# Performance work log

Measured on AMD Instinct MI355X. Metric: run time of the kernel, lower is better.

## Reference

```python
import jax, jax.numpy as jnp
import numpy as np

N, NFEAT, NHID, NCLASS, NHEAD = 8192, 512, 64, 16, 4
ALPHA = 0.1  # leaky relu slope
NEG = -9e15


def setup_inputs() -> dict:
    key = jax.random.key(0)
    ks = jax.random.split(key, 7)
    x = jax.random.normal(ks[0], (N, NFEAT), dtype=jnp.float32)
    adj = (jax.random.uniform(ks[1], (N, N)) < 0.05).astype(jnp.float32)
    # per-head params: W [H, nfeat, nhid], a [H, 2*nhid] (xavier-ish scale)
    W = jax.random.normal(ks[2], (NHEAD, NFEAT, NHID), dtype=jnp.float32) * (1.0 / np.sqrt(NFEAT))
    a = jax.random.normal(ks[3], (NHEAD, 2 * NHID), dtype=jnp.float32) * (1.0 / np.sqrt(NHID))
    W_out = jax.random.normal(ks[4], (NHEAD * NHID, NCLASS), dtype=jnp.float32) * (1.0 / np.sqrt(NHEAD * NHID))
    a_out = jax.random.normal(ks[5], (2 * NCLASS,), dtype=jnp.float32) * (1.0 / np.sqrt(NCLASS))
    return {"x": x, "adj": adj, "W": W, "a": a, "W_out": W_out, "a_out": a_out}


def _gat_layer(h, adj, Wk, ak):
    """Dense pyGAT GraphAttentionLayer (eval mode, dropout = identity)."""
    d = Wk.shape[1]
    Wh = h @ Wk                         # [N, d]
    f1 = Wh @ ak[:d]                    # [N]
    f2 = Wh @ ak[d:]                    # [N]
    e = jax.nn.leaky_relu(f1[:, None] + f2[None, :], negative_slope=ALPHA)  # [N, N]
    att = jax.nn.softmax(jnp.where(adj > 0, e, NEG), axis=1)
    return att @ Wh                     # [N, d]


def reference(x, adj, W, a, W_out, a_out):
    # eval mode: F.dropout is identity
    heads = jax.vmap(lambda Wk, ak: jax.nn.elu(_gat_layer(x, adj, Wk, ak)))(W, a)  # [H, N, nhid]
    h = jnp.transpose(heads, (1, 0, 2)).reshape(x.shape[0], -1)                    # [N, H*nhid]
    out = jax.nn.elu(_gat_layer(h, adj, W_out, a_out))                             # [N, nclass]
    return jax.nn.log_softmax(out, axis=1)
```

## Files before the change

### kernel.cpp

```cpp
#include <hip/hip_runtime.h>
#include <hip/hip_bf16.h>

#define NN 8192
#define NFEAT 512
#define NHID 64
#define NCLASS 16
#define NHEAD 4
#define ALPHA 0.1f
#define CAP 768

typedef short bf16x8 __attribute__((ext_vector_type(8)));
typedef float f32x4 __attribute__((ext_vector_type(4)));
typedef float fv4 __attribute__((ext_vector_type(4)));

__device__ __forceinline__ float lrelu(float x) { return fmaxf(x, ALPHA * x); }
__device__ __forceinline__ float elu(float x) { return x > 0.f ? x : __expf(x) - 1.f; }
__device__ __forceinline__ short f2b(float x) {
  union { __bf16 b; short s; } c; c.b = (__bf16)x; return c.s;
}
__device__ __forceinline__ float b2f(short x) {
  union { unsigned int u; float f; } c; c.u = ((unsigned int)(unsigned short)x) << 16; return c.f;
}

#define UPF(w, v, A0, A1)                                  \
  {                                                        \
    const float lo_ = __uint_as_float((v) << 16);          \
    const float hi_ = __uint_as_float((v) & 0xffff0000u);  \
    (A0) += (w) * lo_;                                     \
    (A1) += (w) * hi_;                                     \
  }

__global__ __launch_bounds__(256) void k_wprep(const float* __restrict__ W,
                                               short* __restrict__ WB) {
  __shared__ float t[64][65];
  const int h = blockIdx.y;
  const int k0 = blockIdx.x * 64;
  const int tid = threadIdx.x;
#pragma unroll
  for (int it = 0; it < 16; ++it) {
    const int r = it * 4 + (tid >> 6), c = tid & 63;
    t[r][c] = W[((size_t)h * NFEAT + k0 + r) * NHID + c];
  }
  __syncthreads();
#pragma unroll
  for (int it = 0; it < 16; ++it) {
    const int d = it * 4 + (tid >> 6), k = tid & 63;
    WB[((size_t)h * NHID + d) * NFEAT + k0 + k] = f2b(t[k][d]);
  }
}

__global__ __launch_bounds__(256) void k_prep1(const float* __restrict__ x,
                                               const short* __restrict__ WB,
                                               const float* __restrict__ a,
                                               short* __restrict__ WhB,
                                               float* __restrict__ f1i,
                                               float* __restrict__ f2i) {
  __shared__ short tile[64][72];
  const int bid = blockIdx.x;
  const int h = bid >> 7;
  const int bm = (bid & 127) * 64;
  const int tid = threadIdx.x;
  const int wv = tid >> 6, lane = tid & 63;
  const int mr = lane & 15, kg = lane >> 4;
  f32x4 acc0 = {0.f, 0.f, 0.f, 0.f}, acc1 = acc0, acc2 = acc0, acc3 = acc0;
  const float* ap = x + (size_t)(bm + wv * 16 + mr) * NFEAT + kg * 8;
  const short* bp = WB + ((size_t)h * NHID + mr) * NFEAT + kg * 8;
#pragma unroll 2
  for (int k0 = 0; k0 < NFEAT; k0 += 32) {
    const float4 xa = *reinterpret_cast<const float4*>(ap);
    const float4 xb = *reinterpret_cast<const float4*>(ap + 4);
    bf16x8 af;
    af[0] = f2b(xa.x); af[1] = f2b(xa.y); af[2] = f2b(xa.z); af[3] = f2b(xa.w);
    af[4] = f2b(xb.x); af[5] = f2b(xb.y); af[6] = f2b(xb.z); af[7] = f2b(xb.w);
    const bf16x8 b0 = *reinterpret_cast<const bf16x8*>(bp);
    const bf16x8 b1 = *reinterpret_cast<const bf16x8*>(bp + 16 * NFEAT);
    const bf16x8 b2 = *reinterpret_cast<const bf16x8*>(bp + 32 * NFEAT);
    const bf16x8 b3 = *reinterpret_cast<const bf16x8*>(bp + 48 * NFEAT);
    acc0 = __builtin_amdgcn_mfma_f32_16x16x32_bf16(af, b0, acc0, 0, 0, 0);
    acc1 = __builtin_amdgcn_mfma_f32_16x16x32_bf16(af, b1, acc1, 0, 0, 0);
    acc2 = __builtin_amdgcn_mfma_f32_16x16x32_bf16(af, b2, acc2, 0, 0, 0);
    acc3 = __builtin_amdgcn_mfma_f32_16x16x32_bf16(af, b3, acc3, 0, 0, 0);
    ap += 32; bp += 32;
  }
  float a1v[4], a2v[4];
#pragma unroll
  for (int c = 0; c < 4; ++c) {
    a1v[c] = a[h * 128 + mr + c * 16];
    a2v[c] = a[h * 128 + 64 + mr + c * 16];
  }
#pragma unroll
  for (int q = 0; q < 4; ++q) {
    float s1 = acc0[q] * a1v[0] + acc1[q] * a1v[1] + acc2[q] * a1v[2] + acc3[q] * a1v[3];
    float s2 = acc0[q] * a2v[0] + acc1[q] * a2v[1] + acc2[q] * a2v[2] + acc3[q] * a2v[3];
#pragma unroll
    for (int off = 1; off < 16; off <<= 1) {
      s1 += __shfl_xor(s1, off);
      s2 += __shfl_xor(s2, off);
    }
    if (mr == 0) {
      const int i = bm + wv * 16 + kg * 4 + q;
      f1i[(size_t)i * 4 + h] = s1;
      f2i[(size_t)i * 4 + h] = s2;
    }
  }
#pragma unroll
  for (int q = 0; q < 4; ++q) {
    const int r = wv * 16 + kg * 4 + q;
    tile[r][mr +  0] = f2b(acc0[q]);
    tile[r][mr + 16] = f2b(acc1[q]);
    tile[r][mr + 32] = f2b(acc2[q]);
    tile[r][mr + 48] = f2b(acc3[q]);
  }
  __syncthreads();
  {
    const int row = tid >> 2, seg = tid & 3;
    bf16x8 o0, o1;
#pragma unroll
    for (int u = 0; u < 8; ++u) {
      o0[u] = tile[row][seg * 16 + u];
      o1[u] = tile[row][seg * 16 + 8 + u];
    }
    short* dst = WhB + (size_t)(bm + row) * 256 + h * 64 + seg * 16;
    *reinterpret_cast<bf16x8*>(dst) = o0;
    *reinterpret_cast<bf16x8*>(dst + 8) = o1;
  }
}

__global__ __launch_bounds__(256) void k_rmax(const float* __restrict__ src,
                                              float* __restrict__ dst, int n, int stride,
                                              int boff) {
  const float* p = src + (size_t)blockIdx.x * boff;
  float m = -1e30f;
  for (int k = threadIdx.x; k < n; k += 256) m = fmaxf(m, p[(size_t)k * stride]);
#pragma unroll
  for (int off = 32; off; off >>= 1) m = fmaxf(m, __shfl_xor(m, off));
  __shared__ float sm[4];
  if ((threadIdx.x & 63) == 0) sm[threadIdx.x >> 6] = m;
  __syncthreads();
  if (threadIdx.x == 0) dst[blockIdx.x] = fmaxf(fmaxf(sm[0], sm[1]), fmaxf(sm[2], sm[3]));
}

__global__ __launch_bounds__(256) void k_scan(const float* __restrict__ adj,
                                              unsigned int* __restrict__ bmask) {
  const fv4* a4 = reinterpret_cast<const fv4*>(adj);
  const int t0 = blockIdx.x * 256 + threadIdx.x;
#pragma unroll 4
  for (int it = 0; it < 32; ++it) {
    const int g = it * 524288 + t0;
    const fv4 v = __builtin_nontemporal_load(a4 + g);
    unsigned int nv = (unsigned int)((v.x > 0.f) | ((v.y > 0.f) << 1) |
                                     ((v.z > 0.f) << 2) | ((v.w > 0.f) << 3))
                      << ((threadIdx.x & 7) * 4);
    nv |= __shfl_xor(nv, 1);
    nv |= __shfl_xor(nv, 2);
    nv |= __shfl_xor(nv, 4);
    if ((threadIdx.x & 7) == 0) bmask[g >> 3] = nv;
  }
}

__global__ __launch_bounds__(256) void k_attn1b(const unsigned int* __restrict__ bmask,
                                                const short* __restrict__ WhB,
                                                const float* __restrict__ f1i,
                                                const float* __restrict__ f2i,
                                                const float* __restrict__ f2max,
                                                short* __restrict__ hcat) {
  __shared__ unsigned short idx[CAP];
  __shared__ unsigned int widx[NHEAD][CAP + 32];
  __shared__ float swred[4][NHEAD];
  __shared__ float sinv[NHEAD];
  __shared__ int cnt;
  const int i = blockIdx.x;
  const int tid = threadIdx.x;
  const int wv = tid >> 6, lane = tid & 63;
  if (tid == 0) cnt = 0;
  __syncthreads();

  {
    unsigned int word = bmask[(size_t)i * 256 + tid];
    const int c = __popc(word);
    if (c) {
      int base = atomicAdd(&cnt, c);
      const int j0 = tid * 32;
      while (word) {
        const int b = __ffs(word) - 1;
        word &= word - 1;
        if (base < CAP) idx[base++] = (unsigned short)(j0 + b);
      }
    }
  }
  __syncthreads();
  const int n = min(cnt, CAP);

  if (tid < 128) widx[tid >> 5][n + (tid & 31)] = 0;

  const float4 f1v = *reinterpret_cast<const float4*>(f1i + (size_t)i * 4);
  const float4 fmx = *reinterpret_cast<const float4*>(f2max);
  float f1r[4], mrow[4], sw[4] = {0.f, 0.f, 0.f, 0.f};
  f1r[0] = f1v.x; f1r[1] = f1v.y; f1r[2] = f1v.z; f1r[3] = f1v.w;
  mrow[0] = lrelu(f1r[0] + fmx.x);
  mrow[1] = lrelu(f1r[1] + fmx.y);
  mrow[2] = lrelu(f1r[2] + fmx.z);
  mrow[3] = lrelu(f1r[3] + fmx.w);
  const float4* f2i4 = reinterpret_cast<const float4*>(f2i);
  for (int k = tid; k < n; k += 256) {
    const int j = idx[k];
    const float4 f = f2i4[j];
    const float w0 = __expf(lrelu(f1r[0] + f.x) - mrow[0]);
    const float w1 = __expf(lrelu(f1r[1] + f.y) - mrow[1]);
    const float w2 = __expf(lrelu(f1r[2] + f.z) - mrow[2]);
    const float w3 = __expf(lrelu(f1r[3] + f.w) - mrow[3]);
    widx[0][k] = ((unsigned int)(unsigned short)f2b(w0) << 16) | (unsigned int)j;
    widx[1][k] = ((unsigned int)(unsigned short)f2b(w1) << 16) | (unsigned int)j;
    widx[2][k] = ((unsigned int)(unsigned short)f2b(w2) << 16) | (unsigned int)j;
    widx[3][k] = ((unsigned int)(unsigned short)f2b(w3) << 16) | (unsigned int)j;
    sw[0] += w0; sw[1] += w1; sw[2] += w2; sw[3] += w3;
  }
#pragma unroll
  for (int off = 32; off; off >>= 1)
#pragma unroll
    for (int h = 0; h < NHEAD; ++h) sw[h] += __shfl_xor(sw[h], off);
  if (lane == 0) {
#pragma unroll
    for (int h = 0; h < NHEAD; ++h) swred[wv][h] = sw[h];
  }
  __syncthreads();
  if (tid < NHEAD) sinv[tid] = 1.f / (swred[0][tid] + swred[1][tid] + swred[2][tid] + swred[3][tid]);

  const int grp = lane >> 4, l = lane & 15;
  float acc0 = 0.f, acc1 = 0.f, acc2 = 0.f, acc3 = 0.f;
  const short* wb = WhB + wv * 64 + l * 4;
  const unsigned int* wrow = widx[wv];
  __syncthreads();
  for (int kb = grp * 8; kb < n; kb += 32) {
    const uint4 pa = *reinterpret_cast<const uint4*>(wrow + kb);
    const uint4 pb = *reinterpret_cast<const uint4*>(wrow + kb + 4);
    const uint2 e0 = *reinterpret_cast<const uint2*>(wb + (size_t)(pa.x & 0xffffu) * 256);
    const uint2 e1 = *reinterpret_cast<const uint2*>(wb + (size_t)(pa.y & 0xffffu) * 256);
    const uint2 e2 = *reinterpret_cast<const uint2*>(wb + (size_t)(pa.z & 0xffffu) * 256);
    const uint2 e3 = *reinterpret_cast<const uint2*>(wb + (size_t)(pa.w & 0xffffu) * 256);
    const uint2 e4 = *reinterpret_cast<const uint2*>(wb + (size_t)(pb.x & 0xffffu) * 256);
    const uint2 e5 = *reinterpret_cast<const uint2*>(wb + (size_t)(pb.y & 0xffffu) * 256);
    const uint2 e6 = *reinterpret_cast<const uint2*>(wb + (size_t)(pb.z & 0xffffu) * 256);
    const uint2 e7 = *reinterpret_cast<const uint2*>(wb + (size_t)(pb.w & 0xffffu) * 256);
    const float w0 = __uint_as_float(pa.x & 0xffff0000u);
    const float w1 = __uint_as_float(pa.y & 0xffff0000u);
    const float w2 = __uint_as_float(pa.z & 0xffff0000u);
    const float w3 = __uint_as_float(pa.w & 0xffff0000u);
    const float w4 = __uint_as_float(pb.x & 0xffff0000u);
    const float w5 = __uint_as_float(pb.y & 0xffff0000u);
    const float w6 = __uint_as_float(pb.z & 0xffff0000u);
    const float w7 = __uint_as_float(pb.w & 0xffff0000u);
    UPF(w0, e0.x, acc0, acc1) UPF(w0, e0.y, acc2, acc3)
    UPF(w1, e1.x, acc0, acc1) UPF(w1, e1.y, acc2, acc3)
    UPF(w2, e2.x, acc0, acc1) UPF(w2, e2.y, acc2, acc3)
    UPF(w3, e3.x, acc0, acc1) UPF(w3, e3.y, acc2, acc3)
    UPF(w4, e4.x, acc0, acc1) UPF(w4, e4.y, acc2, acc3)
    UPF(w5, e5.x, acc0, acc1) UPF(w5, e5.y, acc2, acc3)
    UPF(w6, e6.x, acc0, acc1) UPF(w6, e6.y, acc2, acc3)
    UPF(w7, e7.x, acc0, acc1) UPF(w7, e7.y, acc2, acc3)
  }
  acc0 += __shfl_xor(acc0, 16); acc0 += __shfl_xor(acc0, 32);
  acc1 += __shfl_xor(acc1, 16); acc1 += __shfl_xor(acc1, 32);
  acc2 += __shfl_xor(acc2, 16); acc2 += __shfl_xor(acc2, 32);
  acc3 += __shfl_xor(acc3, 16); acc3 += __shfl_xor(acc3, 32);
  if (lane < 16) {
    const float iv = sinv[wv];
    uint2 o;
    o.x = ((unsigned int)(unsigned short)f2b(elu(acc1 * iv)) << 16) |
          (unsigned int)(unsigned short)f2b(elu(acc0 * iv));
    o.y = ((unsigned int)(unsigned short)f2b(elu(acc3 * iv)) << 16) |
          (unsigned int)(unsigned short)f2b(elu(acc2 * iv));
    *reinterpret_cast<uint2*>(hcat + (size_t)i * 256 + wv * 64 + lane * 4) = o;
  }
}

__global__ __launch_bounds__(256) void k_gemm2(const short* __restrict__ hcat,
                                               const float* __restrict__ Wout,
                                               const float* __restrict__ aout,
                                               short* __restrict__ Wh2B,
                                               float* __restrict__ f1o,
                                               float* __restrict__ f2o) {
  __shared__ float sW[NHEAD * NHID][NCLASS + 1];
  __shared__ float sh[16][NHEAD * NHID + 1];
  const int tid = threadIdx.x;
  const int r = tid >> 4, c = tid & 15;
  const int row = blockIdx.x * 16 + r;
  for (int u = tid; u < 256 * 16; u += 256) sW[u >> 4][u & 15] = Wout[u];
  for (int u = tid; u < 16 * 256; u += 256)
    sh[u >> 8][u & 255] = b2f(hcat[(size_t)(blockIdx.x * 16 + (u >> 8)) * 256 + (u & 255)]);
  __syncthreads();
  float acc = 0.f;
#pragma unroll 8
  for (int f = 0; f < 256; ++f) acc += sh[r][f] * sW[f][c];
  Wh2B[(size_t)row * NCLASS + c] = f2b(acc);
  float s1 = acc * aout[c];
  float s2 = acc * aout[NCLASS + c];
#pragma unroll
  for (int off = 8; off; off >>= 1) { s1 += __shfl_xor(s1, off); s2 += __shfl_xor(s2, off); }
  if (c == 0) { f1o[row] = s1; f2o[row] = s2; }
}

__global__ __launch_bounds__(256) void k_attn2(const unsigned int* __restrict__ bmask,
                                               const short* __restrict__ Wh2B,
                                               const float* __restrict__ f1o,
                                               const float* __restrict__ f2o,
                                               const float* __restrict__ f2omax,
                                               float* __restrict__ out) {
  __shared__ unsigned short idx[CAP];
  __shared__ unsigned int wj[CAP + 4];
  __shared__ float red[4][NCLASS];
  __shared__ float swp[4];
  __shared__ float sinvs;
  __shared__ int cnt;
  const int i = blockIdx.x;
  const int tid = threadIdx.x;
  const int wv = tid >> 6, lane = tid & 63;
  if (tid == 0) cnt = 0;
  __syncthreads();

  {
    unsigned int word = bmask[(size_t)i * 256 + tid];
    const int c = __popc(word);
    if (c) {
      int base = atomicAdd(&cnt, c);
      const int j0 = tid * 32;
      while (word) {
        const int b = __ffs(word) - 1;
        word &= word - 1;
        if (base < CAP) idx[base++] = (unsigned short)(j0 + b);
      }
    }
  }
  __syncthreads();
  const int n = min(cnt, CAP);
  if (tid < 4) wj[n + tid] = 0;

  const float f1r = f1o[i];
  const float mrow = lrelu(f1r + f2omax[0]);
  float sw = 0.f;
  for (int k = tid; k < n; k += 256) {
    const int j = idx[k];
    const float w = __expf(lrelu(f1r + f2o[j]) - mrow);
    wj[k] = ((unsigned int)(unsigned short)f2b(w) << 16) | (unsigned int)j;
    sw += w;
  }
#pragma unroll
  for (int off = 32; off; off >>= 1) sw += __shfl_xor(sw, off);
  if (lane == 0) swp[wv] = sw;
  __syncthreads();
  if (tid == 0) sinvs = 1.f / (swp[0] + swp[1] + swp[2] + swp[3]);
  __syncthreads();

  const int grp = tid >> 2, gl = tid & 3;
  float acc0 = 0.f, acc1 = 0.f, acc2 = 0.f, acc3 = 0.f;
  const short* wb = Wh2B + gl * 4;
  for (int kb = grp * 4; kb < n; kb += 256) {
    const uint4 pw = *reinterpret_cast<const uint4*>(wj + kb);
    const uint2 e0 = *reinterpret_cast<const uint2*>(wb + (size_t)(pw.x & 0xffffu) * NCLASS);
    const uint2 e1 = *reinterpret_cast<const uint2*>(wb + (size_t)(pw.y & 0xffffu) * NCLASS);
    const uint2 e2 = *reinterpret_cast<const uint2*>(wb + (size_t)(pw.z & 0xffffu) * NCLASS);
    const uint2 e3 = *reinterpret_cast<const uint2*>(wb + (size_t)(pw.w & 0xffffu) * NCLASS);
    const float w0 = __uint_as_float(pw.x & 0xffff0000u);
    const float w1 = __uint_as_float(pw.y & 0xffff0000u);
    const float w2 = __uint_as_float(pw.z & 0xffff0000u);
    const float w3 = __uint_as_float(pw.w & 0xffff0000u);
    UPF(w0, e0.x, acc0, acc1) UPF(w0, e0.y, acc2, acc3)
    UPF(w1, e1.x, acc0, acc1) UPF(w1, e1.y, acc2, acc3)
    UPF(w2, e2.x, acc0, acc1) UPF(w2, e2.y, acc2, acc3)
    UPF(w3, e3.x, acc0, acc1) UPF(w3, e3.y, acc2, acc3)
  }
  acc0 += __shfl_xor(acc0, 4);  acc1 += __shfl_xor(acc1, 4);
  acc2 += __shfl_xor(acc2, 4);  acc3 += __shfl_xor(acc3, 4);
  acc0 += __shfl_xor(acc0, 8);  acc1 += __shfl_xor(acc1, 8);
  acc2 += __shfl_xor(acc2, 8);  acc3 += __shfl_xor(acc3, 8);
  acc0 += __shfl_xor(acc0, 16); acc1 += __shfl_xor(acc1, 16);
  acc2 += __shfl_xor(acc2, 16); acc3 += __shfl_xor(acc3, 16);
  acc0 += __shfl_xor(acc0, 32); acc1 += __shfl_xor(acc1, 32);
  acc2 += __shfl_xor(acc2, 32); acc3 += __shfl_xor(acc3, 32);
  if (lane < 4) {
    red[wv][lane * 4 + 0] = acc0;
    red[wv][lane * 4 + 1] = acc1;
    red[wv][lane * 4 + 2] = acc2;
    red[wv][lane * 4 + 3] = acc3;
  }
  __syncthreads();
  if (tid < NCLASS) {
    const float s = red[0][tid] + red[1][tid] + red[2][tid] + red[3][tid];
    const float v = elu(s * sinvs);
    float vm = v;
#pragma unroll
    for (int off = 8; off; off >>= 1) vm = fmaxf(vm, __shfl_xor(vm, off, 16));
    float ex = __expf(v - vm);
#pragma unroll
    for (int off = 8; off; off >>= 1) ex += __shfl_xor(ex, off, 16);
    out[(size_t)i * NCLASS + tid] = v - vm - __logf(ex);
  }
}

extern "C" void kernel_launch(void* const* d_in, const int* in_sizes, int n_in,
                              void* d_out, int out_size, void* d_ws, size_t ws_size,
                              hipStream_t stream) {
  const float* x    = (const float*)d_in[0];
  const float* adj  = (const float*)d_in[1];
  const float* W    = (const float*)d_in[2];
  const float* a    = (const float*)d_in[3];
  const float* Wout = (const float*)d_in[4];
  const float* aout = (const float*)d_in[5];
  float* out = (float*)d_out;
  char* ws = (char*)d_ws;
  const size_t MB = 1048576;

  unsigned int* bmask  = (unsigned int*)(ws);
  short* WhB           = (short*)(ws + 8 * MB);
  short* hcat          = (short*)(ws + 12 * MB);
  short* WB            = (short*)(ws + 16 * MB);
  float* f1i           = (float*)(ws + 16 * MB + 262144);
  float* f2i           = (float*)(ws + 16 * MB + 393216);
  float* f1o           = (float*)(ws + 16 * MB + 524288);
  float* f2o           = (float*)(ws + 16 * MB + 557056);
  short* Wh2B          = (short*)(ws + 16 * MB + 589824);
  float* f2max         = (float*)(ws + 16 * MB + 851968);
  float* f2omax        = (float*)(ws + 16 * MB + 852032);

  k_wprep<<<dim3(8, 4), 256, 0, stream>>>(W, WB);
  k_prep1<<<512, 256, 0, stream>>>(x, WB, a, WhB, f1i, f2i);
  k_rmax<<<NHEAD, 256, 0, stream>>>(f2i, f2max, NN, 4, 1);
  k_scan<<<2048, 256, 0, stream>>>(adj, bmask);
  k_attn1b<<<NN, 256, 0, stream>>>(bmask, WhB, f1i, f2i, f2max, hcat);
  k_gemm2<<<NN / 16, 256, 0, stream>>>(hcat, Wout, aout, Wh2B, f1o, f2o);
  k_rmax<<<1, 256, 0, stream>>>(f2o, f2omax, NN, 1, 0);
  k_attn2<<<NN, 256, 0, stream>>>(bmask, Wh2B, f1o, f2o, f2omax, out);
}
```

Baseline: 243.6 us.

## Split first-layer attention across head pairs with per-pair Wh layout

Launches the first attention kernel on a 2D grid where each block handles one row and a pair of heads. Wh is stored as two separate [N,128] slabs so each gathered row is 256 bytes and the per-pair working set is smaller and more cache friendly. Two waves share each head and split the neighbor list, then combine partial sums through shared memory. The cost is that the adjacency bitmask expansion and index compaction now run twice per row, plus an extra barrier and shared reduction.

```diff
diff --git a/kernel.cpp b/kernel.cpp
--- a/kernel.cpp
+++ b/kernel.cpp
@@ -52,7 +52,7 @@
 __global__ __launch_bounds__(256) void k_prep1(const float* __restrict__ x,
                                                const short* __restrict__ WB,
                                                const float* __restrict__ a,
-                                               short* __restrict__ WhB,
+                                               short* __restrict__ WhB2,
                                                float* __restrict__ f1i,
                                                float* __restrict__ f2i) {
   __shared__ short tile[64][72];
@@ -120,7 +120,8 @@
       o0[u] = tile[row][seg * 16 + u];
       o1[u] = tile[row][seg * 16 + 8 + u];
     }
-    short* dst = WhB + (size_t)(bm + row) * 256 + h * 64 + seg * 16;
+    short* dst = WhB2 + (size_t)(h >> 1) * NN * 128 + (size_t)(bm + row) * 128 +
+                 (h & 1) * 64 + seg * 16;
     *reinterpret_cast<bf16x8*>(dst) = o0;
     *reinterpret_cast<bf16x8*>(dst + 8) = o1;
   }
@@ -158,18 +159,20 @@
   }
 }
 
-__global__ __launch_bounds__(256) void k_attn1b(const unsigned int* __restrict__ bmask,
-                                                const short* __restrict__ WhB,
+__global__ __launch_bounds__(256) void k_attn1h(const unsigned int* __restrict__ bmask,
+                                                const short* __restrict__ WhB2,
                                                 const float* __restrict__ f1i,
                                                 const float* __restrict__ f2i,
                                                 const float* __restrict__ f2max,
                                                 short* __restrict__ hcat) {
   __shared__ unsigned short idx[CAP];
-  __shared__ unsigned int widx[NHEAD][CAP + 32];
-  __shared__ float swred[4][NHEAD];
-  __shared__ float sinv[NHEAD];
+  __shared__ unsigned int widx[2][CAP + 32];
+  __shared__ float red[4][64];
+  __shared__ float swred[4][2];
+  __shared__ float sinv[2];
   __shared__ int cnt;
   const int i = blockIdx.x;
+  const int p = blockIdx.y;
   const int tid = threadIdx.x;
   const int wv = tid >> 6, lane = tid & 63;
   if (tid == 0) cnt = 0;
@@ -191,57 +194,45 @@
   __syncthreads();
   const int n = min(cnt, CAP);
 
-  if (tid < 128) widx[tid >> 5][n + (tid & 31)] = 0;
-
-  const float4 f1v = *reinterpret_cast<const float4*>(f1i + (size_t)i * 4);
-  const float4 fmx = *reinterpret_cast<const float4*>(f2max);
-  float f1r[4], mrow[4], sw[4] = {0.f, 0.f, 0.f, 0.f};
-  f1r[0] = f1v.x; f1r[1] = f1v.y; f1r[2] = f1v.z; f1r[3] = f1v.w;
-  mrow[0] = lrelu(f1r[0] + fmx.x);
-  mrow[1] = lrelu(f1r[1] + fmx.y);
-  mrow[2] = lrelu(f1r[2] + fmx.z);
-  mrow[3] = lrelu(f1r[3] + fmx.w);
-  const float4* f2i4 = reinterpret_cast<const float4*>(f2i);
+  if (tid < 64) widx[tid >> 5][n + (tid & 31)] = 0;
+
+  const float f1r0 = f1i[(size_t)i * 4 + p * 2];
+  const float f1r1 = f1i[(size_t)i * 4 + p * 2 + 1];
+  const float mrow0 = lrelu(f1r0 + f2max[p * 2]);
+  const float mrow1 = lrelu(f1r1 + f2max[p * 2 + 1]);
+  float sw0 = 0.f, sw1 = 0.f;
   for (int k = tid; k < n; k += 256) {
     const int j = idx[k];
-    const float4 f = f2i4[j];
-    const float w0 = __expf(lrelu(f1r[0] + f.x) - mrow[0]);
-    const float w1 = __expf(lrelu(f1r[1] + f.y) - mrow[1]);
-    const float w2 = __expf(lrelu(f1r[2] + f.z) - mrow[2]);
-    const float w3 = __expf(lrelu(f1r[3] + f.w) - mrow[3]);
+    const float2 f = *reinterpret_cast<const float2*>(f2i + (size_t)j * 4 + p * 2);
+    const float w0 = __expf(lrelu(f1r0 + f.x) - mrow0);
+    const float w1 = __expf(lrelu(f1r1 + f.y) - mrow1);
     widx[0][k] = ((unsigned int)(unsigned short)f2b(w0) << 16) | (unsigned int)j;
     widx[1][k] = ((unsigned int)(unsigned short)f2b(w1) << 16) | (unsigned int)j;
-    widx[2][k] = ((unsigned int)(unsigned short)f2b(w2) << 16) | (unsigned int)j;
-    widx[3][k] = ((unsigned int)(unsigned short)f2b(w3) << 16) | (unsigned int)j;
-    sw[0] += w0; sw[1] += w1; sw[2] += w2; sw[3] += w3;
-  }
-#pragma unroll
-  for (int off = 32; off; off >>= 1)
-#pragma unroll
-    for (int h = 0; h < NHEAD; ++h) sw[h] += __shfl_xor(sw[h], off);
-  if (lane == 0) {
-#pragma unroll
-    for (int h = 0; h < NHEAD; ++h) swred[wv][h] = sw[h];
-  }
-  __syncthreads();
-  if (tid < NHEAD) sinv[tid] = 1.f / (swred[0][tid] + swred[1][tid] + swred[2][tid] + swred[3][tid]);
-
+    sw0 += w0; sw1 += w1;
+  }
+#pragma unroll
+  for (int off = 32; off; off >>= 1) { sw0 += __shfl_xor(sw0, off); sw1 += __shfl_xor(sw1, off); }
+  if (lane == 0) { swred[wv][0] = sw0; swred[wv][1] = sw1; }
+  __syncthreads();
+  if (tid < 2) sinv[tid] = 1.f / (swred[0][tid] + swred[1][tid] + swred[2][tid] + swred[3][tid]);
+
+  const int hl = wv >> 1, half = wv & 1;
   const int grp = lane >> 4, l = lane & 15;
   float acc0 = 0.f, acc1 = 0.f, acc2 = 0.f, acc3 = 0.f;
-  const short* wb = WhB + wv * 64 + l * 4;
-  const unsigned int* wrow = widx[wv];
-  __syncthreads();
-  for (int kb = grp * 8; kb < n; kb += 32) {
+  const short* wb = WhB2 + (size_t)p * NN * 128 + hl * 64 + l * 4;
+  const unsigned int* wrow = widx[hl];
+  __syncthreads();
+  for (int kb = (half * 4 + grp) * 8; kb < n; kb += 64) {
     const uint4 pa = *reinterpret_cast<const uint4*>(wrow + kb);
     const uint4 pb = *reinterpret_cast<const uint4*>(wrow + kb + 4);
-    const uint2 e0 = *reinterpret_cast<const uint2*>(wb + (size_t)(pa.x & 0xffffu) * 256);
-    const uint2 e1 = *reinterpret_cast<const uint2*>(wb + (size_t)(pa.y & 0xffffu) * 256);
-    const uint2 e2 = *reinterpret_cast<const uint2*>(wb + (size_t)(pa.z & 0xffffu) * 256);
-    const uint2 e3 = *reinterpret_cast<const uint2*>(wb + (size_t)(pa.w & 0xffffu) * 256);
-    const uint2 e4 = *reinterpret_cast<const uint2*>(wb + (size_t)(pb.x & 0xffffu) * 256);
-    const uint2 e5 = *reinterpret_cast<const uint2*>(wb + (size_t)(pb.y & 0xffffu) * 256);
-    const uint2 e6 = *reinterpret_cast<const uint2*>(wb + (size_t)(pb.z & 0xffffu) * 256);
-    const uint2 e7 = *reinterpret_cast<const uint2*>(wb + (size_t)(pb.w & 0xffffu) * 256);
+    const uint2 e0 = *reinterpret_cast<const uint2*>(wb + (size_t)(pa.x & 0xffffu) * 128);
+    const uint2 e1 = *reinterpret_cast<const uint2*>(wb + (size_t)(pa.y & 0xffffu) * 128);
+    const uint2 e2 = *reinterpret_cast<const uint2*>(wb + (size_t)(pa.z & 0xffffu) * 128);
+    const uint2 e3 = *reinterpret_cast<const uint2*>(wb + (size_t)(pa.w & 0xffffu) * 128);
+    const uint2 e4 = *reinterpret_cast<const uint2*>(wb + (size_t)(pb.x & 0xffffu) * 128);
+    const uint2 e5 = *reinterpret_cast<const uint2*>(wb + (size_t)(pb.y & 0xffffu) * 128);
+    const uint2 e6 = *reinterpret_cast<const uint2*>(wb + (size_t)(pb.z & 0xffffu) * 128);
+    const uint2 e7 = *reinterpret_cast<const uint2*>(wb + (size_t)(pb.w & 0xffffu) * 128);
     const float w0 = __uint_as_float(pa.x & 0xffff0000u);
     const float w1 = __uint_as_float(pa.y & 0xffff0000u);
     const float w2 = __uint_as_float(pa.z & 0xffff0000u);
@@ -264,13 +255,16 @@
   acc2 += __shfl_xor(acc2, 16); acc2 += __shfl_xor(acc2, 32);
   acc3 += __shfl_xor(acc3, 16); acc3 += __shfl_xor(acc3, 32);
   if (lane < 16) {
-    const float iv = sinv[wv];
-    uint2 o;
-    o.x = ((unsigned int)(unsigned short)f2b(elu(acc1 * iv)) << 16) |
-          (unsigned int)(unsigned short)f2b(elu(acc0 * iv));
-    o.y = ((unsigned int)(unsigned short)f2b(elu(acc3 * iv)) << 16) |
-          (unsigned int)(unsigned short)f2b(elu(acc2 * iv));
-    *reinterpret_cast<uint2*>(hcat + (size_t)i * 256 + wv * 64 + lane * 4) = o;
+    red[wv][l * 4 + 0] = acc0;
+    red[wv][l * 4 + 1] = acc1;
+    red[wv][l * 4 + 2] = acc2;
+    red[wv][l * 4 + 3] = acc3;
+  }
+  __syncthreads();
+  if (tid < 128) {
+    const int sub = tid >> 6, d = tid & 63;
+    const float s = red[sub * 2][d] + red[sub * 2 + 1][d];
+    hcat[(size_t)i * 256 + p * 128 + sub * 64 + d] = f2b(elu(s * sinv[sub]));
   }
 }
 
@@ -411,7 +405,7 @@
   const size_t MB = 1048576;
 
   unsigned int* bmask  = (unsigned int*)(ws);
-  short* WhB           = (short*)(ws + 8 * MB);
+  short* WhB2          = (short*)(ws + 8 * MB);
   short* hcat          = (short*)(ws + 12 * MB);
   short* WB            = (short*)(ws + 16 * MB);
   float* f1i           = (float*)(ws + 16 * MB + 262144);
@@ -423,10 +417,10 @@
   float* f2omax        = (float*)(ws + 16 * MB + 852032);
 
   k_wprep<<<dim3(8, 4), 256, 0, stream>>>(W, WB);
-  k_prep1<<<512, 256, 0, stream>>>(x, WB, a, WhB, f1i, f2i);
+  k_prep1<<<512, 256, 0, stream>>>(x, WB, a, WhB2, f1i, f2i);
   k_rmax<<<NHEAD, 256, 0, stream>>>(f2i, f2max, NN, 4, 1);
   k_scan<<<2048, 256, 0, stream>>>(adj, bmask);
-  k_attn1b<<<NN, 256, 0, stream>>>(bmask, WhB, f1i, f2i, f2max, hcat);
+  k_attn1h<<<dim3(NN, 2), 256, 0, stream>>>(bmask, WhB2, f1i, f2i, f2max, hcat);
   k_gemm2<<<NN / 16, 256, 0, stream>>>(hcat, Wout, aout, Wh2B, f1o, f2o);
   k_rmax<<<1, 256, 0, stream>>>(f2o, f2omax, NN, 1, 0);
   k_attn2<<<NN, 256, 0, stream>>>(bmask, Wh2B, f1o, f2o, f2omax, out);
```

Measured after the change: 247.2 us. Within noise of the previous version (+1.5%).
